# Kernel tuning notes

Measured on AMD Instinct MI355X. Metric: run time of the kernel, lower is better.

The kernel has to match this reference:

```python
import jax, jax.numpy as jnp
import numpy as np
from jax import lax

B, C, H, W = 32, 256, 56, 56
OUT_C, K, M = 256, 3, 8
STRIDE = (1, 1)
PADDING = ((1, 1), (1, 1))


def setup_inputs() -> dict:
    key = jax.random.key(0)
    ks = jax.random.split(key, 5)
    x = jax.random.normal(ks[0], (B, C, H, W), dtype=jnp.float32)
    # expert kernels: (M, out_C, in_C/groups, kh, kw), init like torch.randn*0.02
    weight = jax.random.normal(ks[1], (M, OUT_C, C, K, K), dtype=jnp.float32) * 0.02
    bias = jnp.zeros((M, OUT_C), dtype=jnp.float32)
    # gate Linear(in=C, out=M): torch stores weight as (out, in)
    bound = 1.0 / np.sqrt(C)
    gate_w = jax.random.uniform(ks[2], (M, C), minval=-bound, maxval=bound, dtype=jnp.float32)
    gate_b = jax.random.uniform(ks[3], (M,), minval=-bound, maxval=bound, dtype=jnp.float32)
    return {"x": x, "weight": weight, "bias": bias, "gate_w": gate_w, "gate_b": gate_b}


def reference(x, weight, bias, gate_w, gate_b):
    # global average pool -> gating
    gap = jnp.mean(x, axis=(2, 3))                         # (B, C)
    alpha = jax.nn.softmax(gap @ gate_w.T + gate_b, axis=1)  # (B, M)
    # per-sample combined kernels and biases
    kernels = jnp.einsum('bm,moikl->boikl', alpha, weight)  # (B, O, I, k, k)
    biases = alpha @ bias                                   # (B, O)

    def conv_one(xi, wi):
        # xi: (C,H,W), wi: (O,I,k,k)
        out = lax.conv_general_dilated(
            xi[None], wi,
            window_strides=STRIDE, padding=PADDING,
            dimension_numbers=('NCHW', 'OIHW', 'NCHW'))
        return out[0]  # (O, H, W)

    out = jax.vmap(conv_one)(x, kernels)                    # (B, O, H, W)
    return out + biases[:, :, None, None]
```

## Files before the change

kernel.cpp:

```cpp
#include <hip/hip_runtime.h>
#include <hip/hip_bf16.h>

#define B_    32
#define C_    256
#define HW_   3136
#define OC_   256
#define M_    8
#define KPB_  589824

typedef short v8s __attribute__((ext_vector_type(8)));
typedef float f32x4 __attribute__((ext_vector_type(4)));

__device__ __forceinline__ void gll16(const short* src, short* dst) {
    __builtin_amdgcn_global_load_lds((const __attribute__((address_space(1))) void*)src,
                                     (__attribute__((address_space(3))) void*)dst, 16, 0, 0);
}

__global__ void zero_gap_kernel(float* __restrict__ gap) {
    gap[blockIdx.x * 256 + threadIdx.x] = 0.f;
}

__global__ __launch_bounds__(256) void xcast_kernel(const float* __restrict__ x,
                                                    __hip_bfloat16* __restrict__ xg,
                                                    float* __restrict__ gap) {
    __shared__ __hip_bfloat16 tile[64][65];
    int b = blockIdx.z, ct = blockIdx.y, pt = blockIdx.x;
    int p0 = pt*64, c0 = ct*64;
    int tp = threadIdx.x & 63, tc = threadIdx.x >> 6;
    const float* xb = x + ((size_t)b*C_ + c0) * HW_ + p0;
    #pragma unroll
    for (int j = 0; j < 16; ++j) {
        int cl = tc + j*4;
        float v = xb[(size_t)cl*HW_ + tp];
        tile[cl][tp] = __float2bfloat16(v);
        float s = v;
        #pragma unroll
        for (int off = 32; off; off >>= 1) s += __shfl_xor(s, off, 64);
        if (tp == 0) atomicAdd(&gap[b*C_ + c0 + cl], s);
    }
    __syncthreads();
    #pragma unroll
    for (int j = 0; j < 16; ++j) {
        int pl = tc + j*4;
        int p  = p0 + pl;
        int c  = c0 + tp;
        xg[(((size_t)b*8 + (c>>5))*HW_ + p)*32 + (c & 31)] = tile[tp][pl];
    }
}

__global__ void alpha_kernel(const float* __restrict__ gap,
                             const float* __restrict__ gate_w,
                             const float* __restrict__ gate_b,
                             float* __restrict__ alpha) {
    int b = blockIdx.x, lane = threadIdx.x;
    const float inv = 1.0f / HW_;
    float g0 = gap[b*C_ + lane]*inv,       g1 = gap[b*C_ + 64 + lane]*inv;
    float g2 = gap[b*C_ + 128 + lane]*inv, g3 = gap[b*C_ + 192 + lane]*inv;
    float logit[M_];
    #pragma unroll
    for (int m = 0; m < M_; ++m) {
        const float* w = gate_w + m*C_;
        float s = g0*w[lane] + g1*w[64+lane] + g2*w[128+lane] + g3*w[192+lane];
        for (int off = 32; off; off >>= 1) s += __shfl_xor(s, off, 64);
        logit[m] = s + gate_b[m];
    }
    float mx = logit[0];
    #pragma unroll
    for (int m = 1; m < M_; ++m) mx = fmaxf(mx, logit[m]);
    float den = 0.f, e[M_];
    #pragma unroll
    for (int m = 0; m < M_; ++m) { e[m] = __expf(logit[m] - mx); den += e[m]; }
    float mine = 0.f;
    #pragma unroll
    for (int m = 0; m < M_; ++m) if (lane == m) mine = e[m];
    if (lane < M_) alpha[b*M_ + lane] = mine / den;
}

__global__ void biasc_kernel(const float* __restrict__ bias,
                             const float* __restrict__ alpha,
                             float* __restrict__ biasc) {
    int b = blockIdx.x, o = threadIdx.x;
    float s = 0.f;
    #pragma unroll
    for (int m = 0; m < M_; ++m) s += alpha[b*M_+m] * bias[m*OC_+o];
    biasc[b*OC_+o] = s;
}

__global__ __launch_bounds__(256) void combine_kernel(const float* __restrict__ weight,
                                                      const float* __restrict__ alpha,
                                                      __hip_bfloat16* __restrict__ wl) {
    __shared__ float as[B_*M_];
    as[threadIdx.x] = alpha[threadIdx.x];
    __syncthreads();
    int g    = blockIdx.x*256 + threadIdx.x;
    int i_in = g & 31;
    int o    = (g >> 5) & 255;
    int t2   = g >> 13;
    int tap  = t2 % 9;
    int ib   = t2 / 9;
    int i    = ib*32 + i_in;
    int base = o*2304 + i*9 + tap;
    float wv[M_];
    #pragma unroll
    for (int m = 0; m < M_; ++m) wv[m] = weight[(size_t)m*589824 + base];
    for (int b = 0; b < B_; ++b) {
        float s = 0.f;
        #pragma unroll
        for (int m = 0; m < M_; ++m) s += as[b*M_+m] * wv[m];
        wl[(size_t)b*KPB_ + g] = __float2bfloat16(s);
    }
}

__global__ __launch_bounds__(256, 3) void conv_kernel(const short* __restrict__ xg,
                                                      const short* __restrict__ wl,
                                                      const float* __restrict__ biasc,
                                                      float* __restrict__ out) {
    __shared__ short smem[2][8192];
    const int b = blockIdx.z, ot = blockIdx.y, pt = blockIdx.x;
    const int tid = threadIdx.x;
    const int wave = tid >> 6, lane = tid & 63, q = lane >> 4, ln = lane & 15;
    const int o_half = wave >> 1, p_half = wave & 1;
    const int p_base = pt*128 + p_half*64;

    const int DOFF[9] = {-57,-56,-55,-1,0,1,55,56,57};

    unsigned vmask[4]; int p_lane[4];
    #pragma unroll
    for (int c = 0; c < 4; ++c) {
        int p = p_base + c*16 + ln;
        p_lane[c] = p;
        int h = p/56, w = p%56;
        unsigned m = 0;
        #pragma unroll
        for (int tap = 0; tap < 9; ++tap) {
            int h2 = h + tap/3 - 1, w2 = w + tap%3 - 1;
            if ((unsigned)h2 < 56u && (unsigned)w2 < 56u) m |= (1u << tap);
        }
        vmask[c] = m;
    }

    const short* wbase = wl + (size_t)b*KPB_ + (size_t)ot*4096 + tid*8;
    const short* xbase = xg + (size_t)(b*8)*HW_*32 + tid*8;

    auto stage = [&](int kidx, int ib, int doff, int buf) {
        const short* asrc = wbase + (size_t)kidx*8192;
        gll16(asrc,        &smem[buf][tid*8]);
        gll16(asrc + 2048, &smem[buf][tid*8 + 2048]);
        const short* bsrc = xbase + ((long)ib*HW_ + pt*128 + doff)*32;
        gll16(bsrc,        &smem[buf][4096 + tid*8]);
        gll16(bsrc + 2048, &smem[buf][4096 + tid*8 + 2048]);
    };

    f32x4 acc[4][4];
    #pragma unroll
    for (int r = 0; r < 4; ++r)
        #pragma unroll
        for (int c = 0; c < 4; ++c) acc[r][c] = (f32x4){0.f,0.f,0.f,0.f};

    const int aoff = (o_half*64 + ln)*32 + q*8;
    const int boff = 4096 + (p_half*64 + ln)*32 + q*8;
    const v8s vzero = {};

    stage(0, 0, DOFF[0], 0);

    for (int ib = 0; ib < 8; ++ib) {
        #pragma unroll
        for (int tap = 0; tap < 9; ++tap) {
            const int k = ib*9 + tap;
            const int cur = k & 1;
            __syncthreads();
            if (k + 1 < 72) {
                int tap2 = (tap == 8) ? 0 : tap + 1;
                int ib2  = (tap == 8) ? ib + 1 : ib;
                stage(k + 1, ib2, DOFF[tap2], cur ^ 1);
            }
            const short* sm = smem[cur];
            v8s a[4], bf[4];
            #pragma unroll
            for (int r = 0; r < 4; ++r) a[r] = *(const v8s*)(sm + aoff + r*512);
            #pragma unroll
            for (int c = 0; c < 4; ++c) {
                v8s v = *(const v8s*)(sm + boff + c*512);
                bf[c] = ((vmask[c] >> tap) & 1) ? v : vzero;
            }
            #pragma unroll
            for (int r = 0; r < 4; ++r)
                #pragma unroll
                for (int c = 0; c < 4; ++c)
                    acc[r][c] = __builtin_amdgcn_mfma_f32_16x16x32_bf16(a[r], bf[c], acc[r][c], 0, 0, 0);
        }
    }

    const int o_block = ot*128 + o_half*64;
    #pragma unroll
    for (int c = 0; c < 4; ++c) {
        int p = p_lane[c];
        if (p >= HW_) continue;
        float* op = out + (size_t)b * OC_ * HW_ + p;
        #pragma unroll
        for (int r = 0; r < 4; ++r) {
            int o0 = o_block + r*16 + q*4;
            #pragma unroll
            for (int reg = 0; reg < 4; ++reg) {
                int o = o0 + reg;
                op[(size_t)o * HW_] = acc[r][c][reg] + biasc[b*OC_ + o];
            }
        }
    }
}

extern "C" void kernel_launch(void* const* d_in, const int* in_sizes, int n_in,
                              void* d_out, int out_size, void* d_ws, size_t ws_size,
                              hipStream_t stream) {
    const float* x      = (const float*)d_in[0];
    const float* weight = (const float*)d_in[1];
    const float* bias   = (const float*)d_in[2];
    const float* gate_w = (const float*)d_in[3];
    const float* gate_b = (const float*)d_in[4];
    float* out = (float*)d_out;

    char* ws = (char*)d_ws;
    float*          gap   = (float*)(ws);
    float*          biasc = (float*)(ws + 32768);
    float*          alpha = (float*)(ws + 65536);
    __hip_bfloat16* xg    = (__hip_bfloat16*)(ws + 131072);
    __hip_bfloat16* wl    = (__hip_bfloat16*)(ws + 51511296);

    zero_gap_kernel<<<32, 256, 0, stream>>>(gap);
    xcast_kernel   <<<dim3(49, 4, 32), 256, 0, stream>>>(x, xg, gap);
    alpha_kernel   <<<32,  64, 0, stream>>>(gap, gate_w, gate_b, alpha);
    biasc_kernel   <<<32, 256, 0, stream>>>(bias, alpha, biasc);
    combine_kernel <<<2304, 256, 0, stream>>>(weight, alpha, wl);
    conv_kernel    <<<dim3(25, 2, 32), 256, 0, stream>>>((const short*)xg, (const short*)wl, biasc, out);
}
```

Measured before the change: 399.9 us.

## Reuse per-ib input halo tile across all nine taps, widen pixel tile, vectorize stores

```diff
diff --git a/kernel.cpp b/kernel.cpp
--- a/kernel.cpp
+++ b/kernel.cpp
@@ -11,6 +11,8 @@
 typedef short v8s __attribute__((ext_vector_type(8)));
 typedef float f32x4 __attribute__((ext_vector_type(4)));
 
+union bf8pack { v8s v; __hip_bfloat16 h[8]; };
+
 __device__ __forceinline__ void gll16(const short* src, short* dst) {
     __builtin_amdgcn_global_load_lds((const __attribute__((address_space(1))) void*)src,
                                      (__attribute__((address_space(3))) void*)dst, 16, 0, 0);
@@ -21,7 +23,7 @@
 }
 
 __global__ __launch_bounds__(256) void xcast_kernel(const float* __restrict__ x,
-                                                    __hip_bfloat16* __restrict__ xg,
+                                                    short* __restrict__ xg,
                                                     float* __restrict__ gap) {
     __shared__ __hip_bfloat16 tile[64][65];
     int b = blockIdx.z, ct = blockIdx.y, pt = blockIdx.x;
@@ -40,18 +42,24 @@
     }
     __syncthreads();
     #pragma unroll
-    for (int j = 0; j < 16; ++j) {
-        int pl = tc + j*4;
-        int p  = p0 + pl;
-        int c  = c0 + tp;
-        xg[(((size_t)b*8 + (c>>5))*HW_ + p)*32 + (c & 31)] = tile[tp][pl];
+    for (int it = 0; it < 2; ++it) {
+        int idx = it*256 + threadIdx.x;
+        int px = idx >> 3, ck = idx & 7;
+        bf8pack pk;
+        #pragma unroll
+        for (int j = 0; j < 8; ++j) pk.h[j] = tile[ck*8 + j][px];
+        int c = c0 + ck*8;
+        size_t dst = (((size_t)b*8 + (c >> 5))*HW_ + p0 + px)*32 + (c & 31);
+        *(v8s*)(xg + dst) = pk.v;
     }
 }
 
 __global__ void alpha_kernel(const float* __restrict__ gap,
                              const float* __restrict__ gate_w,
                              const float* __restrict__ gate_b,
-                             float* __restrict__ alpha) {
+                             const float* __restrict__ bias,
+                             float* __restrict__ alpha,
+                             float* __restrict__ biasc) {
     int b = blockIdx.x, lane = threadIdx.x;
     const float inv = 1.0f / HW_;
     float g0 = gap[b*C_ + lane]*inv,       g1 = gap[b*C_ + 64 + lane]*inv;
@@ -70,64 +78,69 @@
     float den = 0.f, e[M_];
     #pragma unroll
     for (int m = 0; m < M_; ++m) { e[m] = __expf(logit[m] - mx); den += e[m]; }
-    float mine = 0.f;
-    #pragma unroll
-    for (int m = 0; m < M_; ++m) if (lane == m) mine = e[m];
-    if (lane < M_) alpha[b*M_ + lane] = mine / den;
-}
-
-__global__ void biasc_kernel(const float* __restrict__ bias,
-                             const float* __restrict__ alpha,
-                             float* __restrict__ biasc) {
-    int b = blockIdx.x, o = threadIdx.x;
-    float s = 0.f;
-    #pragma unroll
-    for (int m = 0; m < M_; ++m) s += alpha[b*M_+m] * bias[m*OC_+o];
-    biasc[b*OC_+o] = s;
+    float am[M_];
+    #pragma unroll
+    for (int m = 0; m < M_; ++m) am[m] = e[m] / den;
+    if (lane < M_) alpha[b*M_ + lane] = am[lane];
+    #pragma unroll
+    for (int r = 0; r < 4; ++r) {
+        int o = r*64 + lane;
+        float s = 0.f;
+        #pragma unroll
+        for (int m = 0; m < M_; ++m) s += am[m] * bias[m*OC_ + o];
+        biasc[b*OC_ + o] = s;
+    }
 }
 
 __global__ __launch_bounds__(256) void combine_kernel(const float* __restrict__ weight,
                                                       const float* __restrict__ alpha,
-                                                      __hip_bfloat16* __restrict__ wl) {
+                                                      short* __restrict__ wl) {
     __shared__ float as[B_*M_];
     as[threadIdx.x] = alpha[threadIdx.x];
     __syncthreads();
-    int g    = blockIdx.x*256 + threadIdx.x;
-    int i_in = g & 31;
-    int o    = (g >> 5) & 255;
-    int t2   = g >> 13;
-    int tap  = t2 % 9;
-    int ib   = t2 / 9;
-    int i    = ib*32 + i_in;
-    int base = o*2304 + i*9 + tap;
-    float wv[M_];
-    #pragma unroll
-    for (int m = 0; m < M_; ++m) wv[m] = weight[(size_t)m*589824 + base];
+    int gc  = blockIdx.x*256 + threadIdx.x;
+    int i8  = gc & 3;
+    int o   = (gc >> 2) & 255;
+    int t2  = gc >> 10;
+    int tap = t2 % 9;
+    int ib  = t2 / 9;
+    int base = o*2304 + (ib*32 + i8*8)*9 + tap;
+    float wv[M_][8];
+    #pragma unroll
+    for (int m = 0; m < M_; ++m)
+        #pragma unroll
+        for (int j = 0; j < 8; ++j)
+            wv[m][j] = weight[(size_t)m*589824 + base + j*9];
     for (int b = 0; b < B_; ++b) {
-        float s = 0.f;
-        #pragma unroll
-        for (int m = 0; m < M_; ++m) s += as[b*M_+m] * wv[m];
-        wl[(size_t)b*KPB_ + g] = __float2bfloat16(s);
-    }
-}
-
-__global__ __launch_bounds__(256, 3) void conv_kernel(const short* __restrict__ xg,
+        bf8pack pk;
+        #pragma unroll
+        for (int j = 0; j < 8; ++j) {
+            float s = 0.f;
+            #pragma unroll
+            for (int m = 0; m < M_; ++m) s += as[b*M_+m] * wv[m][j];
+            pk.h[j] = __float2bfloat16(s);
+        }
+        *(v8s*)(wl + (size_t)b*KPB_ + (size_t)gc*8) = pk.v;
+    }
+}
+
+__global__ __launch_bounds__(256, 2) void conv_kernel(const short* __restrict__ xg,
                                                       const short* __restrict__ wl,
                                                       const float* __restrict__ biasc,
                                                       float* __restrict__ out) {
-    __shared__ short smem[2][8192];
+    __shared__ short smem[32768];
     const int b = blockIdx.z, ot = blockIdx.y, pt = blockIdx.x;
     const int tid = threadIdx.x;
     const int wave = tid >> 6, lane = tid & 63, q = lane >> 4, ln = lane & 15;
     const int o_half = wave >> 1, p_half = wave & 1;
-    const int p_base = pt*128 + p_half*64;
+    const int P0 = pt*256;
 
     const int DOFF[9] = {-57,-56,-55,-1,0,1,55,56,57};
 
-    unsigned vmask[4]; int p_lane[4];
-    #pragma unroll
-    for (int c = 0; c < 4; ++c) {
-        int p = p_base + c*16 + ln;
+    unsigned vmask[8]; int p_lane[8];
+    #pragma unroll
+    for (int c = 0; c < 8; ++c) {
+        int p = P0 + p_half*128 + c*16 + ln;
         p_lane[c] = p;
         int h = p/56, w = p%56;
         unsigned m = 0;
@@ -139,61 +152,62 @@
         vmask[c] = m;
     }
 
-    const short* wbase = wl + (size_t)b*KPB_ + (size_t)ot*4096 + tid*8;
-    const short* xbase = xg + (size_t)(b*8)*HW_*32 + tid*8;
-
-    auto stage = [&](int kidx, int ib, int doff, int buf) {
-        const short* asrc = wbase + (size_t)kidx*8192;
-        gll16(asrc,        &smem[buf][tid*8]);
-        gll16(asrc + 2048, &smem[buf][tid*8 + 2048]);
-        const short* bsrc = xbase + ((long)ib*HW_ + pt*128 + doff)*32;
-        gll16(bsrc,        &smem[buf][4096 + tid*8]);
-        gll16(bsrc + 2048, &smem[buf][4096 + tid*8 + 2048]);
+    const short* wbase = wl + (size_t)b*KPB_ + ot*4096 + tid*8;
+    const short* xbase = xg + (size_t)(b*8)*HW_*32;
+
+    auto stageA = [&](int kidx, int buf) {
+        const short* src = wbase + (size_t)kidx*8192;
+        gll16(src,        &smem[buf*4096 + tid*8]);
+        gll16(src + 2048, &smem[buf*4096 + tid*8 + 2048]);
     };
-
-    f32x4 acc[4][4];
+    auto stageB = [&](int ib, int buf) {
+        const short* src = xbase + ((long)ib*HW_ + P0 - 64)*32 + tid*8;
+        short* dst = &smem[8192 + buf*12288 + tid*8];
+        #pragma unroll
+        for (int r = 0; r < 6; ++r) gll16(src + r*2048, dst + r*2048);
+    };
+
+    f32x4 acc[4][8];
     #pragma unroll
     for (int r = 0; r < 4; ++r)
         #pragma unroll
-        for (int c = 0; c < 4; ++c) acc[r][c] = (f32x4){0.f,0.f,0.f,0.f};
-
-    const int aoff = (o_half*64 + ln)*32 + q*8;
-    const int boff = 4096 + (p_half*64 + ln)*32 + q*8;
+        for (int c = 0; c < 8; ++c) acc[r][c] = (f32x4){0.f,0.f,0.f,0.f};
+
+    stageA(0, 0);
+    stageB(0, 0);
+
+    const int a_lane_off = (o_half*64 + ln)*32 + q*8;
+    const int b_lane_off = (64 + p_half*128 + ln)*32 + q*8;
     const v8s vzero = {};
 
-    stage(0, 0, DOFF[0], 0);
-
     for (int ib = 0; ib < 8; ++ib) {
+        const short* bbuf = &smem[8192 + (ib & 1)*12288 + b_lane_off];
         #pragma unroll
         for (int tap = 0; tap < 9; ++tap) {
             const int k = ib*9 + tap;
-            const int cur = k & 1;
             __syncthreads();
-            if (k + 1 < 72) {
-                int tap2 = (tap == 8) ? 0 : tap + 1;
-                int ib2  = (tap == 8) ? ib + 1 : ib;
-                stage(k + 1, ib2, DOFF[tap2], cur ^ 1);
+            if (k + 1 < 72) stageA(k + 1, (k + 1) & 1);
+            if (tap == 0 && ib < 7) stageB(ib + 1, (ib + 1) & 1);
+
+            const short* am = &smem[(k & 1)*4096 + a_lane_off];
+            v8s a[4];
+            #pragma unroll
+            for (int r = 0; r < 4; ++r) a[r] = *(const v8s*)(am + r*512);
+            const short* bm = bbuf + DOFF[tap]*32;
+            #pragma unroll
+            for (int c = 0; c < 8; ++c) {
+                v8s v = *(const v8s*)(bm + c*512);
+                v8s bf = ((vmask[c] >> tap) & 1) ? v : vzero;
+                #pragma unroll
+                for (int r = 0; r < 4; ++r)
+                    acc[r][c] = __builtin_amdgcn_mfma_f32_16x16x32_bf16(a[r], bf, acc[r][c], 0, 0, 0);
             }
-            const short* sm = smem[cur];
-            v8s a[4], bf[4];
-            #pragma unroll
-            for (int r = 0; r < 4; ++r) a[r] = *(const v8s*)(sm + aoff + r*512);
-            #pragma unroll
-            for (int c = 0; c < 4; ++c) {
-                v8s v = *(const v8s*)(sm + boff + c*512);
-                bf[c] = ((vmask[c] >> tap) & 1) ? v : vzero;
-            }
-            #pragma unroll
-            for (int r = 0; r < 4; ++r)
-                #pragma unroll
-                for (int c = 0; c < 4; ++c)
-                    acc[r][c] = __builtin_amdgcn_mfma_f32_16x16x32_bf16(a[r], bf[c], acc[r][c], 0, 0, 0);
         }
     }
 
     const int o_block = ot*128 + o_half*64;
     #pragma unroll
-    for (int c = 0; c < 4; ++c) {
+    for (int c = 0; c < 8; ++c) {
         int p = p_lane[c];
         if (p >= HW_) continue;
         float* op = out + (size_t)b * OC_ * HW_ + p;
@@ -220,16 +234,15 @@
     float* out = (float*)d_out;
 
     char* ws = (char*)d_ws;
-    float*          gap   = (float*)(ws);
-    float*          biasc = (float*)(ws + 32768);
-    float*          alpha = (float*)(ws + 65536);
-    __hip_bfloat16* xg    = (__hip_bfloat16*)(ws + 131072);
-    __hip_bfloat16* wl    = (__hip_bfloat16*)(ws + 51511296);
+    float* gap   = (float*)(ws);
+    float* biasc = (float*)(ws + 32768);
+    float* alpha = (float*)(ws + 65536);
+    short* xg    = (short*)(ws + 131072);
+    short* wl    = (short*)(ws + 51511296);
 
     zero_gap_kernel<<<32, 256, 0, stream>>>(gap);
     xcast_kernel   <<<dim3(49, 4, 32), 256, 0, stream>>>(x, xg, gap);
-    alpha_kernel   <<<32,  64, 0, stream>>>(gap, gate_w, gate_b, alpha);
-    biasc_kernel   <<<32, 256, 0, stream>>>(bias, alpha, biasc);
-    combine_kernel <<<2304, 256, 0, stream>>>(weight, alpha, wl);
-    conv_kernel    <<<dim3(25, 2, 32), 256, 0, stream>>>((const short*)xg, (const short*)wl, biasc, out);
-}
+    alpha_kernel   <<<32,  64, 0, stream>>>(gap, gate_w, gate_b, bias, alpha, biasc);
+    combine_kernel <<<288, 256, 0, stream>>>(weight, alpha, wl);
+    conv_kernel    <<<dim3(13, 2, 32), 256, 0, stream>>>(xg, wl, biasc, out);
+}
```

Result: no change. 395.2 us (-1.2%).
